# Optimization experiments

Measured on AMD Instinct MI355X. Metric: run time of the kernel, lower is better.

Reference implementation:

```python
import jax, jax.numpy as jnp
import numpy as np

L, T, B, D, H, DQK, DV, FF = 4, 1024, 4, 1024, 16, 64, 64, 4096
EPS = 1e-6


def setup_inputs() -> dict:
    key = jax.random.key(0)
    ks = jax.random.split(key, 11)
    s = 0.02
    f32 = jnp.float32
    return {
        "x": jax.random.normal(ks[0], (T, B, D), f32),
        "mask": jnp.ones((B, T), bool),
        "Wk": jax.random.normal(ks[1], (L, D, H * DQK), f32) * s,
        "bk": jnp.zeros((L, H * DQK), f32),
        "Wq": jax.random.normal(ks[2], (L, D, H * DQK), f32) * s,
        "bq": jnp.zeros((L, H * DQK), f32),
        "Wv": jax.random.normal(ks[3], (L, D, H * DV), f32) * s,
        "bv": jnp.zeros((L, H * DV), f32),
        "W1": jax.random.normal(ks[4], (L, D, FF), f32) * s,
        "b1": jnp.zeros((L, FF), f32),
        "W2": jax.random.normal(ks[5], (L, FF, D), f32) * s,
        "b2": jnp.zeros((L, D), f32),
    }


def _resnorm(x, fx):
    # residual + (x - mean) / (std + eps); torch.std is unbiased (ddof=1)
    y = x + fx
    mu = y.mean(-1, keepdims=True)
    sd = y.std(-1, keepdims=True, ddof=1)
    return (y - mu) / (sd + EPS)


def _ff(x, W1, b1, W2, b2):
    # Feedforward default puts ReLU after every linear layer, including the last
    h = jax.nn.relu(x @ W1 + b1)
    return jax.nn.relu(h @ W2 + b2)


def _attn(x, mask, Wk, bk, Wq, bq, Wv, bv):
    # x: (T, B, D); mask: (B, T)
    k = (x @ Wk + bk).reshape(T, B, H, DQK)
    q = (x @ Wq + bq).reshape(T, B, H, DQK)
    # kern[b,h,i,j] = <key_i, query_j> / sqrt(D)   (note: scaled by model dim D)
    kern = jnp.einsum('ibhj,kbhj->bhik', k, q) / np.sqrt(D)
    kern = jnp.where(mask[:, None, None, :], kern, -jnp.inf)
    A = jax.nn.softmax(kern, axis=-1)  # softmax over query axis (as in source)
    v = (x @ Wv + bv).reshape(T, B, H, DV)
    out = jnp.einsum('bhij,jbhk->ibhk', A, v)  # (T, B, H, DV)
    return out.reshape(T, B, H * DV)


def reference(x, mask, Wk, bk, Wq, bq, Wv, bv, W1, b1, W2, b2):
    for l in range(L):
        z = _resnorm(x, _ff(x, W1[l], b1[l], W2[l], b2[l]))
        x = _resnorm(z, _attn(z, mask, Wk[l], bk[l], Wq[l], bq[l], Wv[l], bv[l]))
    return x
```

## Files before the change

kernel.cpp:

```cpp
#include <hip/hip_runtime.h>
#include <cstdint>
#include <cstddef>

#define TT    1024
#define DD    1024
#define FFD   4096
#define NLAYER 4
#define MROWS 4096

typedef __bf16 bf16;
typedef __bf16 bf16x8 __attribute__((ext_vector_type(8)));
typedef __bf16 bf16x4v __attribute__((ext_vector_type(4)));
typedef float  f32x4  __attribute__((ext_vector_type(4)));

__device__ __forceinline__ bf16 f2b(float f) { return (bf16)f; }

typedef __attribute__((address_space(3))) unsigned int lds_u32;
typedef __attribute__((address_space(1))) const unsigned int g_u32;
__device__ __forceinline__ void gl_lds16(const bf16* g, bf16* l) {
    __builtin_amdgcn_global_load_lds((g_u32*)g, (lds_u32*)l, 16, 0, 0);
}

__global__ __launch_bounds__(256) void cvt_k(const float* __restrict__ src,
                                             bf16* __restrict__ dst) {
    const int i = blockIdx.x * 256 + threadIdx.x;
    f32x4 v = *(const f32x4*)(src + (size_t)i * 4);
    bf16x4v o;
#pragma unroll
    for (int u = 0; u < 4; ++u) o[u] = f2b(v[u]);
    *(bf16x4v*)(dst + (size_t)i * 4) = o;
}

__device__ __forceinline__ void tr_tile(const float* __restrict__ src,
                                        bf16* __restrict__ dst, int R, int C,
                                        int bx, int by, int t) {
    __shared__ bf16 tile[32][33];
    const int tx = t & 31, ty = (t >> 5) * 4;
    const int c0 = bx * 32, r0 = by * 32;
#pragma unroll
    for (int u = 0; u < 4; ++u)
        tile[ty + u][tx] = f2b(src[(size_t)(r0 + ty + u) * C + c0 + tx]);
    __syncthreads();
#pragma unroll
    for (int u = 0; u < 4; ++u)
        dst[(size_t)(c0 + ty + u) * R + r0 + tx] = tile[tx][ty + u];
}

__global__ __launch_bounds__(256) void prep_k(const float* __restrict__ W1,
                                              const float* __restrict__ W2,
                                              const float* __restrict__ Wk,
                                              const float* __restrict__ Wq,
                                              const float* __restrict__ Wv,
                                              const float* __restrict__ bkp,
                                              const float* __restrict__ bqp,
                                              const float* __restrict__ bvp,
                                              bf16* __restrict__ w1t,
                                              bf16* __restrict__ w2t,
                                              bf16* __restrict__ kqvt,
                                              float* __restrict__ bcat) {
    const int id = blockIdx.x, t = threadIdx.x;
    if (id < 4096) {
        tr_tile(W1, w1t, 1024, 4096, id & 127, id >> 7, t);
    } else if (id < 8192) {
        const int r = id - 4096;
        tr_tile(W2, w2t, 4096, 1024, r & 31, r >> 5, t);
    } else if (id < 9216) {
        const int r = id - 8192;
        tr_tile(Wk, kqvt, 1024, 1024, r & 31, r >> 5, t);
    } else if (id < 10240) {
        const int r = id - 9216;
        tr_tile(Wq, kqvt + 1048576, 1024, 1024, r & 31, r >> 5, t);
    } else if (id < 11264) {
        const int r = id - 10240;
        tr_tile(Wv, kqvt + 2097152, 1024, 1024, r & 31, r >> 5, t);
    } else {
        const int i = (id - 11264) * 256 + t;
        bcat[i] = (i < 1024) ? bkp[i] : (i < 2048 ? bqp[i - 1024] : bvp[i - 2048]);
    }
}

__global__ __launch_bounds__(256) void vtrans_k(const bf16* __restrict__ src,
                                                bf16* __restrict__ dst) {
    __shared__ bf16 tile[32][33];
    const int t  = threadIdx.x;
    const int tx = t & 31, ty = (t >> 5) * 4;
    const int bh = blockIdx.z, tt = blockIdx.y * 32, dv0 = blockIdx.x * 32;
    const int b = bh >> 4, h = bh & 15;
#pragma unroll
    for (int u = 0; u < 4; ++u)
        tile[ty + u][tx] = src[(size_t)((tt + ty + u) * 4 + b) * 3072 + h * 64 + dv0 + tx];
    __syncthreads();
#pragma unroll
    for (int u = 0; u < 4; ++u)
        dst[(size_t)(bh * 64 + dv0 + ty + u) * 1024 + tt + tx] = tile[tx][ty + u];
}

template <bool RELU, int BN, bool DBUF>
__global__ __launch_bounds__(256) void gemm_bt(const bf16* __restrict__ A, int lda,
                                               const bf16* __restrict__ Bt, int ldb,
                                               const float* __restrict__ bias,
                                               bf16* __restrict__ C, int ldc, int K) {
    constexpr int WC = (BN == 128) ? 2 : 1;
    constexpr int MW = 128 / (4 / WC);
    constexpr int NW = BN / WC;
    constexpr int MI = MW / 16;
    constexpr int NI = NW / 16;
    constexpr int NB = BN / 32;
    constexpr int NBUF = DBUF ? 2 : 1;
    __shared__ bf16 As[NBUF][128 * 64];
    __shared__ bf16 Bs[NBUF][BN * 64];
    const int t = threadIdx.x;
    const int w = t >> 6, lane = t & 63, l15 = lane & 15, qd = lane >> 4;
    int bid = blockIdx.y * gridDim.x + blockIdx.x;
    {
        const int q = (int)(gridDim.x * gridDim.y) >> 3;
        bid = (bid & 7) * q + (bid >> 3);
    }
    const int bx = bid % (int)gridDim.x, by = bid / (int)gridDim.x;
    const int m0 = by * 128, n0 = bx * BN;
    const int wr = (w / WC) * MW, wc = (w % WC) * NW;
    const int srow = lane >> 3, scol = ((lane & 7) ^ srow) * 8;
    const int sx = (l15 & 7) << 3;
    f32x4 acc[MI][NI] = {};

    auto stage = [&](int buf, int k0) {
#pragma unroll
        for (int i = 0; i < 4; ++i) {
            const int r0 = (w * 4 + i) * 8;
            gl_lds16(A + (size_t)(m0 + r0 + srow) * lda + k0 + scol,
                     &As[buf][0] + r0 * 64 + lane * 8);
        }
#pragma unroll
        for (int i = 0; i < NB; ++i) {
            const int r0 = (w * NB + i) * 8;
            gl_lds16(Bt + (size_t)(n0 + r0 + srow) * ldb + k0 + scol,
                     &Bs[buf][0] + r0 * 64 + lane * 8);
        }
    };
    auto compute = [&](int buf) {
#pragma unroll
        for (int kk = 0; kk < 64; kk += 32) {
            bf16x8 af[MI], bfr[NI];
#pragma unroll
            for (int i = 0; i < MI; ++i)
                af[i] = *(const bf16x8*)(&As[buf][0] + (wr + i * 16 + l15) * 64 + ((kk + qd * 8) ^ sx));
#pragma unroll
            for (int j = 0; j < NI; ++j)
                bfr[j] = *(const bf16x8*)(&Bs[buf][0] + (wc + j * 16 + l15) * 64 + ((kk + qd * 8) ^ sx));
#pragma unroll
            for (int i = 0; i < MI; ++i)
#pragma unroll
                for (int j = 0; j < NI; ++j)
                    acc[i][j] = __builtin_amdgcn_mfma_f32_16x16x32_bf16(af[i], bfr[j], acc[i][j], 0, 0, 0);
        }
    };

    if (DBUF) {
        const int nt = K >> 6;
        int cur = 0;
        stage(0, 0);
        __syncthreads();
        for (int it = 0; it < nt - 1; ++it) {
            stage(cur ^ 1, (it + 1) << 6);
            compute(cur);
            __syncthreads();
            cur ^= 1;
        }
        compute(cur);
    } else {
        for (int k0 = 0; k0 < K; k0 += 64) {
            stage(0, k0);
            __syncthreads();
            compute(0);
            __syncthreads();
        }
    }

#pragma unroll
    for (int j = 0; j < NI; ++j) {
        const int col = n0 + wc + j * 16 + l15;
        const float bz = bias[col];
#pragma unroll
        for (int i = 0; i < MI; ++i) {
            const int row = m0 + wr + i * 16 + qd * 4;
#pragma unroll
            for (int p = 0; p < 4; ++p) {
                float c = acc[i][j][p] + bz;
                if (RELU) c = fmaxf(c, 0.f);
                C[(size_t)(row + p) * ldc + col] = f2b(c);
            }
        }
    }
}

__device__ __forceinline__ float block_sum(float s, float* red, int w, int lane) {
#pragma unroll
    for (int off = 32; off >= 1; off >>= 1) s += __shfl_xor(s, off, 64);
    if (lane == 0) red[w] = s;
    __syncthreads();
    return red[0] + red[1] + red[2] + red[3];
}

template <bool OUT_F32>
__global__ __launch_bounds__(256) void resnorm_k(const bf16* __restrict__ x,
                                                 const bf16* __restrict__ fx,
                                                 void* __restrict__ outv) {
    __shared__ float red1[4], red2[4];
    const int t = threadIdx.x, w = t >> 6, lane = t & 63;
    const size_t base = (size_t)blockIdx.x * DD + t * 4;
    bf16x4v xv = *(const bf16x4v*)(x + base);
    bf16x4v fv = *(const bf16x4v*)(fx + base);
    float y[4], s = 0.f;
#pragma unroll
    for (int u = 0; u < 4; ++u) { y[u] = (float)xv[u] + (float)fv[u]; s += y[u]; }
    s = block_sum(s, red1, w, lane);
    const float mu = s * (1.f / DD);
    float v = 0.f;
#pragma unroll
    for (int u = 0; u < 4; ++u) { const float d = y[u] - mu; v += d * d; }
    v = block_sum(v, red2, w, lane);
    const float sd = sqrtf(v * (1.f / (DD - 1)));
    const float ri = 1.f / (sd + 1e-6f);
    if (OUT_F32) {
        f32x4 ov;
#pragma unroll
        for (int u = 0; u < 4; ++u) ov[u] = (y[u] - mu) * ri;
        *(f32x4*)((float*)outv + base) = ov;
    } else {
        bf16x4v ov;
#pragma unroll
        for (int u = 0; u < 4; ++u) ov[u] = f2b((y[u] - mu) * ri);
        *(bf16x4v*)((bf16*)outv + base) = ov;
    }
}

__global__ __launch_bounds__(256, 2) void attn_k(const bf16* __restrict__ kq,
                                                 const bf16* __restrict__ vt,
                                                 bf16* __restrict__ out) {
    __shared__ bf16 smem[17408 + 9216 + 8704];
    bf16* PlK = smem;
    bf16* Qt  = smem + 17408;
    bf16* Vts = smem + 17408 + 9216;
    const int t = threadIdx.x;
    const int w = t >> 6, lane = t & 63, l15 = lane & 15, qd = lane >> 4;
    int bid = blockIdx.y * 8 + blockIdx.x;
    bid = (bid & 7) * 64 + (bid >> 3);
    const int i0 = (bid & 7) * 128, bh = bid >> 3, b = bh >> 4, h = bh & 15;
    const size_t kbase = (size_t)b * 3072 + h * 64;
    const int sr = t >> 3, sc = (t & 7) * 8;
    const int vr = t >> 2, vc = (t & 3) * 32;
    const float SC = 0.03125f;

#pragma unroll
    for (int ch = 0; ch < 4; ++ch) {
        const int r = ch * 32 + sr;
        *(bf16x8*)(PlK + r * 72 + sc) =
            *(const bf16x8*)(kq + (size_t)(i0 + r) * 12288 + kbase + sc);
    }
    __syncthreads();
    bf16x8 kf[2][2];
#pragma unroll
    for (int i = 0; i < 2; ++i)
#pragma unroll
        for (int kx = 0; kx < 2; ++kx)
            kf[i][kx] = *(const bf16x8*)(PlK + (w * 32 + i * 16 + l15) * 72 + kx * 32 + qd * 8);
    bf16* Pl = PlK + w * 4352;

    f32x4 acc_o[2][4] = {};
    float lsum[2][4] = {};

    for (int j0 = 0; j0 < TT; j0 += 128) {
#pragma unroll
        for (int ch = 0; ch < 4; ++ch) {
            const int r = ch * 32 + sr;
            *(bf16x8*)(Qt + r * 72 + sc) =
                *(const bf16x8*)(kq + (size_t)(j0 + r) * 12288 + kbase + 1024 + sc);
        }
#pragma unroll
        for (int u = 0; u < 4; ++u)
            *(bf16x8*)(Vts + vr * 136 + vc + u * 8) =
                *(const bf16x8*)(vt + (size_t)(bh * 64 + vr) * 1024 + j0 + vc + u * 8);
        __syncthreads();

        f32x4 accs[2][8] = {};
#pragma unroll
        for (int kx = 0; kx < 2; ++kx) {
            bf16x8 bfr[8];
#pragma unroll
            for (int j = 0; j < 8; ++j)
                bfr[j] = *(const bf16x8*)(Qt + (j * 16 + l15) * 72 + kx * 32 + qd * 8);
#pragma unroll
            for (int i = 0; i < 2; ++i)
#pragma unroll
                for (int j = 0; j < 8; ++j)
                    accs[i][j] = __builtin_amdgcn_mfma_f32_16x16x32_bf16(kf[i][kx], bfr[j], accs[i][j], 0, 0, 0);
        }

#pragma unroll
        for (int i = 0; i < 2; ++i)
#pragma unroll
            for (int j = 0; j < 8; ++j)
#pragma unroll
                for (int p = 0; p < 4; ++p) {
                    const float pv = __expf(accs[i][j][p] * SC);
                    lsum[i][p] += pv;
                    Pl[(i * 16 + qd * 4 + p) * 136 + j * 16 + l15] = f2b(pv);
                }

#pragma unroll
        for (int kt = 0; kt < 4; ++kt) {
            bf16x8 pa[2], vb[4];
#pragma unroll
            for (int i = 0; i < 2; ++i)
                pa[i] = *(const bf16x8*)(Pl + (i * 16 + l15) * 136 + kt * 32 + qd * 8);
#pragma unroll
            for (int n = 0; n < 4; ++n)
                vb[n] = *(const bf16x8*)(Vts + (n * 16 + l15) * 136 + kt * 32 + qd * 8);
#pragma unroll
            for (int i = 0; i < 2; ++i)
#pragma unroll
                for (int n = 0; n < 4; ++n)
                    acc_o[i][n] = __builtin_amdgcn_mfma_f32_16x16x32_bf16(pa[i], vb[n], acc_o[i][n], 0, 0, 0);
        }
        __syncthreads();
    }

#pragma unroll
    for (int i = 0; i < 2; ++i)
#pragma unroll
        for (int p = 0; p < 4; ++p) {
            float s = lsum[i][p];
#pragma unroll
            for (int off = 1; off < 16; off <<= 1) s += __shfl_xor(s, off, 64);
            const float ri = 1.f / s;
            const int ig = i0 + w * 32 + i * 16 + qd * 4 + p;
#pragma unroll
            for (int n = 0; n < 4; ++n)
                out[(size_t)ig * 4096 + b * 1024 + h * 64 + n * 16 + l15] = f2b(acc_o[i][n][p] * ri);
        }
}

extern "C" void kernel_launch(void* const* d_in, const int* in_sizes, int n_in,
                              void* d_out, int out_size, void* d_ws, size_t ws_size,
                              hipStream_t stream) {
    const float* x_in = (const float*)d_in[0];
    const float* Wk = (const float*)d_in[2];
    const float* bk = (const float*)d_in[3];
    const float* Wq = (const float*)d_in[4];
    const float* bq = (const float*)d_in[5];
    const float* Wv = (const float*)d_in[6];
    const float* bv = (const float*)d_in[7];
    const float* W1 = (const float*)d_in[8];
    const float* b1 = (const float*)d_in[9];
    const float* W2 = (const float*)d_in[10];
    const float* b2 = (const float*)d_in[11];

    bf16* ws = (bf16*)d_ws;
    const size_t M1 = 1024 * 1024;
    bf16* w1t  = ws;
    bf16* w2t  = ws +  4 * M1;
    bf16* kqvt = ws +  8 * M1;
    bf16* vtb  = ws + 11 * M1;
    bf16* fbuf = ws + 15 * M1;
    bf16* zbuf = ws + 19 * M1;
    bf16* xb   = ws + 23 * M1;
    bf16* big  = ws + 27 * M1;
    float* bcat = (float*)(ws + 43 * M1);
    float* outp = (float*)d_out;

    cvt_k<<<dim3(MROWS * DD / 1024), 256, 0, stream>>>(x_in, xb);

    const bf16* xcur = xb;
    for (int l = 0; l < NLAYER; ++l) {
        prep_k<<<dim3(11276), 256, 0, stream>>>(
            W1 + (size_t)l * DD * FFD, W2 + (size_t)l * FFD * DD,
            Wk + (size_t)l * M1, Wq + (size_t)l * M1, Wv + (size_t)l * M1,
            bk + (size_t)l * DD, bq + (size_t)l * DD, bv + (size_t)l * DD,
            w1t, w2t, kqvt, bcat);
        gemm_bt<true, 128, false><<<dim3(FFD / 128, MROWS / 128), 256, 0, stream>>>(
            xcur, DD, w1t, DD, b1 + (size_t)l * FFD, big, FFD, DD);
        gemm_bt<true, 64, true><<<dim3(DD / 64, MROWS / 128), 256, 0, stream>>>(
            big, FFD, w2t, FFD, b2 + (size_t)l * DD, fbuf, DD, FFD);
        resnorm_k<false><<<dim3(MROWS), 256, 0, stream>>>(xcur, fbuf, zbuf);
        gemm_bt<false, 128, false><<<dim3(3072 / 128, MROWS / 128), 256, 0, stream>>>(
            zbuf, DD, kqvt, DD, bcat, big, 3072, DD);
        vtrans_k<<<dim3(2, 32, 64), 256, 0, stream>>>(big + 2048, vtb);
        attn_k<<<dim3(8, 64), 256, 0, stream>>>(big, vtb, fbuf);
        if (l == NLAYER - 1)
            resnorm_k<true><<<dim3(MROWS), 256, 0, stream>>>(zbuf, fbuf, outp);
        else
            resnorm_k<false><<<dim3(MROWS), 256, 0, stream>>>(zbuf, fbuf, xb);
        xcur = xb;
    }
}
```

Measured before the change: 1.009 ms.

## Use triple-buffered LDS pipeline with vmcnt waits in down-projection GEMM

```diff
diff --git a/kernel.cpp b/kernel.cpp
--- a/kernel.cpp
+++ b/kernel.cpp
@@ -95,7 +95,7 @@
         dst[(size_t)(bh * 64 + dv0 + ty + u) * 1024 + tt + tx] = tile[tx][ty + u];
 }
 
-template <bool RELU, int BN, bool DBUF>
+template <bool RELU, int BN, int NBUF>
 __global__ __launch_bounds__(256) void gemm_bt(const bf16* __restrict__ A, int lda,
                                                const bf16* __restrict__ Bt, int ldb,
                                                const float* __restrict__ bias,
@@ -106,7 +106,7 @@
     constexpr int MI = MW / 16;
     constexpr int NI = NW / 16;
     constexpr int NB = BN / 32;
-    constexpr int NBUF = DBUF ? 2 : 1;
+    static_assert(NBUF == 1 || (NBUF == 3 && BN == 64), "pipeline cfg");
     __shared__ bf16 As[NBUF][128 * 64];
     __shared__ bf16 Bs[NBUF][BN * 64];
     const int t = threadIdx.x;
@@ -155,18 +155,23 @@
         }
     };
 
-    if (DBUF) {
+    if (NBUF == 3) {
         const int nt = K >> 6;
-        int cur = 0;
         stage(0, 0);
-        __syncthreads();
-        for (int it = 0; it < nt - 1; ++it) {
-            stage(cur ^ 1, (it + 1) << 6);
-            compute(cur);
-            __syncthreads();
-            cur ^= 1;
-        }
-        compute(cur);
+        stage(1, 64);
+        for (int it = 0; it < nt; ++it) {
+            if (it + 2 < nt) {
+                stage((it + 2) % 3, (it + 2) << 6);
+                asm volatile("s_waitcnt vmcnt(12)" ::: "memory");
+            } else if (it + 1 < nt) {
+                asm volatile("s_waitcnt vmcnt(6)" ::: "memory");
+            } else {
+                asm volatile("s_waitcnt vmcnt(0)" ::: "memory");
+            }
+            __builtin_amdgcn_s_barrier();
+            compute(it % 3);
+            __builtin_amdgcn_s_barrier();
+        }
     } else {
         for (int k0 = 0; k0 < K; k0 += 64) {
             stage(0, k0);
@@ -377,12 +382,12 @@
             Wk + (size_t)l * M1, Wq + (size_t)l * M1, Wv + (size_t)l * M1,
             bk + (size_t)l * DD, bq + (size_t)l * DD, bv + (size_t)l * DD,
             w1t, w2t, kqvt, bcat);
-        gemm_bt<true, 128, false><<<dim3(FFD / 128, MROWS / 128), 256, 0, stream>>>(
+        gemm_bt<true, 128, 1><<<dim3(FFD / 128, MROWS / 128), 256, 0, stream>>>(
             xcur, DD, w1t, DD, b1 + (size_t)l * FFD, big, FFD, DD);
-        gemm_bt<true, 64, true><<<dim3(DD / 64, MROWS / 128), 256, 0, stream>>>(
+        gemm_bt<true, 64, 3><<<dim3(DD / 64, MROWS / 128), 256, 0, stream>>>(
             big, FFD, w2t, FFD, b2 + (size_t)l * DD, fbuf, DD, FFD);
         resnorm_k<false><<<dim3(MROWS), 256, 0, stream>>>(xcur, fbuf, zbuf);
-        gemm_bt<false, 128, false><<<dim3(3072 / 128, MROWS / 128), 256, 0, stream>>>(
+        gemm_bt<false, 128, 1><<<dim3(3072 / 128, MROWS / 128), 256, 0, stream>>>(
             zbuf, DD, kqvt, DD, bcat, big, 3072, DD);
         vtrans_k<<<dim3(2, 32, 64), 256, 0, stream>>>(big + 2048, vtb);
         attn_k<<<dim3(8, 64), 256, 0, stream>>>(big, vtb, fbuf);
```

Result: no change. 1.002 ms (-0.7%).
